# Optimization experiments

Hardware: AMD Instinct MI355X
Metric: run time of the kernel (lower is better)

## Reference

```python
import jax, jax.numpy as jnp
import numpy as np

N_EMBD = 2048
N_HEAD = 16
N_PREVS = 4
HEAD_DIM = N_EMBD // N_HEAD  # 128
B, T = 4, 2048


def setup_inputs() -> dict:
    key = jax.random.key(0)
    ks = jax.random.split(key, 3 + 2 * N_PREVS)
    inp = {
        "x": jax.random.normal(ks[0], (B, T, N_EMBD), dtype=jnp.float32),
        "w_attn": jax.random.normal(ks[1], (3 * N_EMBD, N_EMBD), dtype=jnp.float32) * 0.02,
        "w_proj": jax.random.normal(ks[2], (N_EMBD, N_EMBD), dtype=jnp.float32) * 0.02,
    }
    for i in range(N_PREVS):
        inp[f"prev_k{i}"] = jax.random.normal(ks[3 + 2 * i], (B, N_HEAD, T, HEAD_DIM), dtype=jnp.float32)
        inp[f"prev_v{i}"] = jax.random.normal(ks[4 + 2 * i], (B, N_HEAD, T, HEAD_DIM), dtype=jnp.float32)
    return inp


def _attn(q, k, v, causal):
    # q,k,v: [B, H, T, D]
    scale = 1.0 / jnp.sqrt(jnp.asarray(q.shape[-1], q.dtype))
    scores = jnp.einsum("bhqd,bhkd->bhqk", q, k) * scale
    if causal:
        mask = jnp.tril(jnp.ones((q.shape[2], k.shape[2]), dtype=bool))
        scores = jnp.where(mask, scores, jnp.finfo(scores.dtype).min)
    p = jax.nn.softmax(scores, axis=-1)
    return jnp.einsum("bhqk,bhkd->bhqd", p, v)


def reference(x, w_attn, w_proj,
              prev_k0, prev_v0, prev_k1, prev_v1,
              prev_k2, prev_v2, prev_k3, prev_v3):
    prevs = [(prev_k0, prev_v0), (prev_k1, prev_v1), (prev_k2, prev_v2), (prev_k3, prev_v3)]
    Bx, Tx, C = x.shape
    qkv = jnp.einsum("btc,fc->btf", x, w_attn)  # [B,T,3C]
    q, k, v = jnp.split(qkv, 3, axis=-1)

    def heads(t):  # [B,T,C] -> [B,H,T,D]
        return t.reshape(Bx, Tx, N_HEAD, HEAD_DIM).transpose(0, 2, 1, 3)

    q, k, v = heads(q), heads(k), heads(v)
    cur_k, cur_v = k, v

    sa_h = N_HEAD - N_PREVS
    # causal self-attention over first sa_h heads
    self_attn = _attn(q[:, :sa_h], k[:, :sa_h], v[:, :sa_h], causal=True)

    # cross-attention: head sa_h+i attends (non-causal) to head sa_h+i of prev layer i's cache
    qc = q[:, sa_h:]
    kc = jnp.stack([pk[:, sa_h + i] for i, (pk, pv) in enumerate(prevs)], axis=1)
    vc = jnp.stack([pv[:, sa_h + i] for i, (pk, pv) in enumerate(prevs)], axis=1)
    cross_attn = _attn(qc, kc, vc, causal=False)

    y = jnp.concatenate([self_attn, cross_attn], axis=1)  # [B,H,T,D]
    y = y.transpose(0, 2, 1, 3).reshape(Bx, Tx, C)
    y = jnp.einsum("btc,oc->bto", y, w_proj)
    return y, cur_k, cur_v
```

## Files before the change

### kernel.cpp

```cpp
#include <hip/hip_runtime.h>
#include <hip/hip_bf16.h>
#include <stdint.h>

typedef __attribute__((ext_vector_type(8))) short short8;
typedef __attribute__((ext_vector_type(4))) float floatx4;

#define NE 2048
#define NH 16
#define HD 128
#define SAH 12
#define BB 4
#define TT 2048
#define MM (BB*TT)
#define NQKV (3*NE)

__device__ __forceinline__ ushort f2bfu(float f){
    __hip_bfloat16 h = __float2bfloat16(f);
    union { __hip_bfloat16 h; ushort u; } c; c.h = h; return c.u;
}

__global__ void cvt_f32_bf16(const float* __restrict__ s, ushort* __restrict__ d, int n4){
    const int stride = gridDim.x * blockDim.x;
    for (int i = blockIdx.x*blockDim.x + threadIdx.x; i < n4; i += stride){
        const float4 v = ((const float4*)s)[i];
        ushort4 o;
        o.x = f2bfu(v.x); o.y = f2bfu(v.y); o.z = f2bfu(v.z); o.w = f2bfu(v.w);
        ((ushort4*)d)[i] = o;
    }
}

template<int MODE>
__global__ __launch_bounds__(256) void gemm_bt(
    const ushort* __restrict__ A, const ushort* __restrict__ Bw,
    ushort* __restrict__ Cbf, float* __restrict__ Cf,
    float* __restrict__ outK, float* __restrict__ outV,
    int N, int K)
{
    __shared__ __align__(16) ushort Alds[128*32];
    __shared__ __align__(16) ushort Blds[128*32];
    const int tid  = threadIdx.x;
    const int wave = tid >> 6, lane = tid & 63;
    const int m0 = blockIdx.y << 7, n0 = blockIdx.x << 7;
    const int wr = wave >> 1, wc = wave & 1;

    floatx4 acc[4][4];
#pragma unroll
    for (int i=0;i<4;i++)
#pragma unroll
        for (int j=0;j<4;j++) acc[i][j] = (floatx4){0.f,0.f,0.f,0.f};

    const int sr = lane >> 2, sc = (lane & 3) << 3;
    const ushort* gA = A  + (size_t)(m0 + wave*32 + sr)*K + sc;
    const ushort* gB = Bw + (size_t)(n0 + wave*32 + sr)*K + sc;
    ushort* lA = Alds + wave*32*32;
    ushort* lB = Blds + wave*32*32;
    const int fr = lane & 15, fo = (lane >> 4) << 3;

    for (int kt = 0; kt < K; kt += 32){
        __builtin_amdgcn_global_load_lds((__attribute__((address_space(1))) void*)(gA + kt),
                                         (__attribute__((address_space(3))) void*)lA, 16, 0, 0);
        __builtin_amdgcn_global_load_lds((__attribute__((address_space(1))) void*)(gA + kt + (size_t)16*K),
                                         (__attribute__((address_space(3))) void*)(lA + 16*32), 16, 0, 0);
        __builtin_amdgcn_global_load_lds((__attribute__((address_space(1))) void*)(gB + kt),
                                         (__attribute__((address_space(3))) void*)lB, 16, 0, 0);
        __builtin_amdgcn_global_load_lds((__attribute__((address_space(1))) void*)(gB + kt + (size_t)16*K),
                                         (__attribute__((address_space(3))) void*)(lB + 16*32), 16, 0, 0);
        __syncthreads();
        short8 af[4], bfb[4];
#pragma unroll
        for (int i=0;i<4;i++) af[i]  = *(const short8*)(Alds + (wr*64 + i*16 + fr)*32 + fo);
#pragma unroll
        for (int j=0;j<4;j++) bfb[j] = *(const short8*)(Blds + (wc*64 + j*16 + fr)*32 + fo);
#pragma unroll
        for (int i=0;i<4;i++)
#pragma unroll
            for (int j=0;j<4;j++)
                acc[i][j] = __builtin_amdgcn_mfma_f32_16x16x32_bf16(af[i], bfb[j], acc[i][j], 0, 0, 0);
        __syncthreads();
    }

#pragma unroll
    for (int i=0;i<4;i++){
#pragma unroll
        for (int j=0;j<4;j++){
#pragma unroll
            for (int r=0;r<4;r++){
                const int row = m0 + wr*64 + i*16 + ((lane>>4)<<2) + r;
                const int col = n0 + wc*64 + j*16 + fr;
                const float v = acc[i][j][r];
                if (MODE == 0){
                    Cf[(size_t)row*N + col] = v;
                } else {
                    Cbf[(size_t)row*NQKV + col] = f2bfu(v);
                    if (col >= NE){
                        const int b = row >> 11, t = row & (TT-1);
                        const int hd = (col - NE) & (NE-1);
                        float* dst = (col >= 2*NE) ? outV : outK;
                        dst[(((size_t)b*NH + (hd>>7))*TT + t)*HD + (hd & 127)] = v;
                    }
                }
            }
        }
    }
}

__global__ __launch_bounds__(256) void attn(
    const ushort* __restrict__ qkv, ushort* __restrict__ Y,
    const float* __restrict__ pk0, const float* __restrict__ pv0,
    const float* __restrict__ pk1, const float* __restrict__ pv1,
    const float* __restrict__ pk2, const float* __restrict__ pv2,
    const float* __restrict__ pk3, const float* __restrict__ pv3)
{
    __shared__ __align__(16) ushort Klds[32*136];
    __shared__ __align__(16) ushort Vt[128*40];
    __shared__ __align__(16) ushort Plds[4][16*40];

    const int tid  = threadIdx.x;
    const int wave = tid >> 6, lane = tid & 63;
    const int bid = blockIdx.x;
    const int qt = bid & 31;
    const int h  = (bid >> 5) & 15;
    const int b  = bid >> 9;
    const int q0 = qt << 6;
    const bool causal = (h < SAH);

    const float* pkc = nullptr; const float* pvc = nullptr;
    if (!causal){
        const int i = h - SAH;
        if      (i==0){ pkc=pk0; pvc=pv0; }
        else if (i==1){ pkc=pk1; pvc=pv1; }
        else if (i==2){ pkc=pk2; pvc=pv2; }
        else          { pkc=pk3; pvc=pv3; }
        const size_t off = ((size_t)b*NH + h)*(size_t)TT*HD;
        pkc += off; pvc += off;
    }

    const int fr = lane & 15, fo = (lane>>4) << 3;
    const int wq = q0 + wave*16;

    short8 qf[4];
    {
        const ushort* qp = qkv + (size_t)(b*TT + wq + fr)*NQKV + h*HD + fo;
#pragma unroll
        for (int kk=0;kk<4;kk++) qf[kk] = *(const short8*)(qp + kk*32);
    }

    floatx4 o[8];
#pragma unroll
    for (int dt=0; dt<8; dt++) o[dt] = (floatx4){0.f,0.f,0.f,0.f};
    float m_run[4] = {-1e30f,-1e30f,-1e30f,-1e30f};
    float l_run[4] = {0.f,0.f,0.f,0.f};

    const int srr = tid >> 3;
    const int sds = (tid & 7) << 4;
    const int nkb = causal ? ((q0 >> 5) + 2) : (TT/32);

    for (int kb = 0; kb < nkb; kb++){
        const int kstart = kb << 5;
        short8 k0v, k1v, v0v, v1v;
        if (causal){
            const ushort* sk = qkv + (size_t)(b*TT + kstart + srr)*NQKV + NE + h*HD + sds;
            const ushort* sv = sk + NE;
            k0v = *(const short8*)sk;     k1v = *(const short8*)(sk+8);
            v0v = *(const short8*)sv;     v1v = *(const short8*)(sv+8);
        } else {
            const float* sk = pkc + (size_t)(kstart + srr)*HD + sds;
            const float* sv = pvc + (size_t)(kstart + srr)*HD + sds;
            ushort* kp = (ushort*)&k0v;  ushort* kp1 = (ushort*)&k1v;
            ushort* vp = (ushort*)&v0v;  ushort* vp1 = (ushort*)&v1v;
#pragma unroll
            for (int e=0;e<8;e++){ kp[e]  = f2bfu(sk[e]);   vp[e]  = f2bfu(sv[e]); }
#pragma unroll
            for (int e=0;e<8;e++){ kp1[e] = f2bfu(sk[8+e]); vp1[e] = f2bfu(sv[8+e]); }
        }
        *(short8*)(Klds + srr*136 + sds)     = k0v;
        *(short8*)(Klds + srr*136 + sds + 8) = k1v;
        {
            const ushort* vp  = (const ushort*)&v0v;
            const ushort* vp1 = (const ushort*)&v1v;
#pragma unroll
            for (int e=0;e<8;e++) Vt[(sds+e)*40 + srr]   = vp[e];
#pragma unroll
            for (int e=0;e<8;e++) Vt[(sds+8+e)*40 + srr] = vp1[e];
        }
        __syncthreads();

        if (!causal || kstart <= wq + 15){
            floatx4 s0 = (floatx4){0.f,0.f,0.f,0.f}, s1 = (floatx4){0.f,0.f,0.f,0.f};
#pragma unroll
            for (int kk=0;kk<4;kk++){
                short8 kb0 = *(const short8*)(Klds + fr*136       + kk*32 + fo);
                short8 kb1 = *(const short8*)(Klds + (16+fr)*136  + kk*32 + fo);
                s0 = __builtin_amdgcn_mfma_f32_16x16x32_bf16(qf[kk], kb0, s0, 0,0,0);
                s1 = __builtin_amdgcn_mfma_f32_16x16x32_bf16(qf[kk], kb1, s1, 0,0,0);
            }
            const float scale = 0.08838834764831845f;
            ushort* Pw = Plds[wave];
#pragma unroll
            for (int r=0;r<4;r++){
                const int qpos = wq + ((lane>>4)<<2) + r;
                float x0 = s0[r]*scale, x1 = s1[r]*scale;
                if (causal){
                    if (kstart + fr      > qpos) x0 = -1e30f;
                    if (kstart + 16 + fr > qpos) x1 = -1e30f;
                }
                float mx = fmaxf(x0, x1);
#pragma unroll
                for (int mmk=1; mmk<16; mmk<<=1) mx = fmaxf(mx, __shfl_xor(mx, mmk));
                mx = fmaxf(mx, m_run[r]);
                const float alpha = __expf(m_run[r] - mx);
                m_run[r] = mx;
                const float p0 = __expf(x0 - mx), p1 = __expf(x1 - mx);
                float ps = p0 + p1;
#pragma unroll
                for (int mmk=1; mmk<16; mmk<<=1) ps += __shfl_xor(ps, mmk);
                l_run[r] = l_run[r]*alpha + ps;
#pragma unroll
                for (int dt=0;dt<8;dt++) o[dt][r] *= alpha;
                const int prow = ((lane>>4)<<2) + r;
                Pw[prow*40 + fr]      = f2bfu(p0);
                Pw[prow*40 + 16 + fr] = f2bfu(p1);
            }
            asm volatile("s_waitcnt lgkmcnt(0)" ::: "memory");
            short8 pf = *(const short8*)(Pw + fr*40 + fo);
#pragma unroll
            for (int dt=0;dt<8;dt++){
                short8 vf = *(const short8*)(Vt + (dt*16 + fr)*40 + fo);
                o[dt] = __builtin_amdgcn_mfma_f32_16x16x32_bf16(pf, vf, o[dt], 0,0,0);
            }
        }
        __syncthreads();
    }

    float inv[4];
#pragma unroll
    for (int r=0;r<4;r++) inv[r] = 1.0f / l_run[r];
#pragma unroll
    for (int dt=0;dt<8;dt++){
#pragma unroll
        for (int r=0;r<4;r++){
            const int q = wq + ((lane>>4)<<2) + r;
            const int d = dt*16 + fr;
            Y[(size_t)(b*TT + q)*NE + h*HD + d] = f2bfu(o[dt][r]*inv[r]);
        }
    }
}

extern "C" void kernel_launch(void* const* d_in, const int* in_sizes, int n_in,
                              void* d_out, int out_size, void* d_ws, size_t ws_size,
                              hipStream_t stream)
{
    const float* x      = (const float*)d_in[0];
    const float* w_attn = (const float*)d_in[1];
    const float* w_proj = (const float*)d_in[2];
    const float* pk0 = (const float*)d_in[3];
    const float* pv0 = (const float*)d_in[4];
    const float* pk1 = (const float*)d_in[5];
    const float* pv1 = (const float*)d_in[6];
    const float* pk2 = (const float*)d_in[7];
    const float* pv2 = (const float*)d_in[8];
    const float* pk3 = (const float*)d_in[9];
    const float* pv3 = (const float*)d_in[10];

    float* outY = (float*)d_out;
    float* outK = outY + (size_t)MM*NE;
    float* outV = outK + (size_t)MM*NE;

    char* w = (char*)d_ws;
    ushort* x_bf   = (ushort*)(w);
    ushort* wa_bf  = (ushort*)(w + 33554432);
    ushort* wp_bf  = (ushort*)(w + 58720256);
    ushort* qkv_bf = (ushort*)(w + 67108864);
    ushort* y_bf   = (ushort*)(w + 167772160);

    cvt_f32_bf16<<<2048, 256, 0, stream>>>(x,      x_bf,  MM*NE/4);
    cvt_f32_bf16<<<2048, 256, 0, stream>>>(w_attn, wa_bf, NQKV*NE/4);
    cvt_f32_bf16<<<1024, 256, 0, stream>>>(w_proj, wp_bf, NE*NE/4);

    gemm_bt<1><<<dim3(NQKV/128, MM/128), 256, 0, stream>>>(
        x_bf, wa_bf, qkv_bf, nullptr, outK, outV, NQKV, NE);

    attn<<<BB*NH*(TT/64), 256, 0, stream>>>(
        qkv_bf, y_bf, pk0, pv0, pk1, pv1, pk2, pv2, pk3, pv3);

    gemm_bt<0><<<dim3(NE/128, MM/128), 256, 0, stream>>>(
        y_bf, wp_bf, nullptr, outY, nullptr, nullptr, NE, NE);
}
```

Before: 1.507 ms.

## Pretranspose V and preconvert cross KV, use 64-key tiles with direct LDS loads

Adds pre-pass kernels that convert the cross-attention K cache to bf16 and write V (self and cross) pre-transposed into workspace buffers reused from the earlier conversion buffers. The attention kernel now processes 64-key blocks, fills LDS with global_load_lds using an XOR swizzle instead of per-element transposing stores, and drops the per-block fp32-to-bf16 conversion of the cross caches. This targets uncoalesced scalar LDS transposes, redundant conversions repeated by each query tile, and sync overhead. The cost is extra kernel launches and transpose passes through global memory. The w_proj conversion moves after attention so its buffer can hold the K cache.

```diff
diff --git a/kernel.cpp b/kernel.cpp
--- a/kernel.cpp
+++ b/kernel.cpp
@@ -13,11 +13,14 @@
 #define TT 2048
 #define MM (BB*TT)
 #define NQKV (3*NE)
+#define KBLK 64
 
 __device__ __forceinline__ ushort f2bfu(float f){
     __hip_bfloat16 h = __float2bfloat16(f);
     union { __hip_bfloat16 h; ushort u; } c; c.h = h; return c.u;
 }
+
+__device__ __forceinline__ int swz(int r){ return (((r>>3)&3)<<1) ^ (r&7); }
 
 __global__ void cvt_f32_bf16(const float* __restrict__ s, ushort* __restrict__ d, int n4){
     const int stride = gridDim.x * blockDim.x;
@@ -27,6 +30,53 @@
         o.x = f2bfu(v.x); o.y = f2bfu(v.y); o.z = f2bfu(v.z); o.w = f2bfu(v.w);
         ((ushort4*)d)[i] = o;
     }
+}
+
+__global__ void kc_cvt(const float* __restrict__ pk0, const float* __restrict__ pk1,
+                       const float* __restrict__ pk2, const float* __restrict__ pk3,
+                       ushort* __restrict__ kc){
+    const int bh2 = blockIdx.y;
+    const int i = bh2 & 3, b = bh2 >> 2;
+    const float* src = (i==0?pk0 : i==1?pk1 : i==2?pk2 : pk3)
+                     + (size_t)(b*NH + SAH + i)*TT*HD;
+    const int idx = (blockIdx.x*256 + threadIdx.x)*8;
+    float4 a0 = *(const float4*)(src + idx);
+    float4 a1 = *(const float4*)(src + idx + 4);
+    ushort* dst = kc + (size_t)bh2*TT*HD + idx;
+    ushort4 o0, o1;
+    o0.x=f2bfu(a0.x); o0.y=f2bfu(a0.y); o0.z=f2bfu(a0.z); o0.w=f2bfu(a0.w);
+    o1.x=f2bfu(a1.x); o1.y=f2bfu(a1.y); o1.z=f2bfu(a1.z); o1.w=f2bfu(a1.w);
+    *(ushort4*)dst = o0; *(ushort4*)(dst+4) = o1;
+}
+
+__global__ void vt_cross_k(const float* __restrict__ pv0, const float* __restrict__ pv1,
+                           const float* __restrict__ pv2, const float* __restrict__ pv3,
+                           ushort* __restrict__ vtC){
+    const int bh2 = blockIdx.z;
+    const int i = bh2 & 3, b = bh2 >> 2;
+    const int db = blockIdx.y;
+    const int t  = blockIdx.x*256 + threadIdx.x;
+    const float* src = (i==0?pv0 : i==1?pv1 : i==2?pv2 : pv3)
+                     + ((size_t)(b*NH + SAH + i)*TT + t)*HD + db*8;
+    float4 a0 = *(const float4*)src;
+    float4 a1 = *(const float4*)(src + 4);
+    float vals[8] = {a0.x,a0.y,a0.z,a0.w,a1.x,a1.y,a1.z,a1.w};
+#pragma unroll
+    for (int e=0;e<8;e++)
+        vtC[((size_t)bh2*HD + db*8 + e)*TT + t] = f2bfu(vals[e]);
+}
+
+__global__ void vt_self_k(const ushort* __restrict__ qkv, ushort* __restrict__ vtS){
+    const int bh = blockIdx.z;
+    const int b = bh/12, h = bh%12;
+    const int db = blockIdx.y;
+    const int t  = blockIdx.x*256 + threadIdx.x;
+    const ushort* src = qkv + (size_t)(b*TT + t)*NQKV + 2*NE + h*HD + db*8;
+    short8 v = *(const short8*)src;
+    const ushort* vp = (const ushort*)&v;
+#pragma unroll
+    for (int e=0;e<8;e++)
+        vtS[((size_t)bh*HD + db*8 + e)*TT + t] = vp[e];
 }
 
 template<int MODE>
@@ -104,19 +154,18 @@
     }
 }
 
-__global__ __launch_bounds__(256) void attn(
-    const ushort* __restrict__ qkv, ushort* __restrict__ Y,
-    const float* __restrict__ pk0, const float* __restrict__ pv0,
-    const float* __restrict__ pk1, const float* __restrict__ pv1,
-    const float* __restrict__ pk2, const float* __restrict__ pv2,
-    const float* __restrict__ pk3, const float* __restrict__ pv3)
+__global__ __launch_bounds__(256) void attn2(
+    const ushort* __restrict__ qkv, const ushort* __restrict__ kc,
+    const ushort* __restrict__ vtS, const ushort* __restrict__ vtC,
+    ushort* __restrict__ Y)
 {
-    __shared__ __align__(16) ushort Klds[32*136];
-    __shared__ __align__(16) ushort Vt[128*40];
-    __shared__ __align__(16) ushort Plds[4][16*40];
+    __shared__ __align__(16) ushort Klds[64*128];
+    __shared__ __align__(16) ushort Vlds[128*64];
+    __shared__ __align__(16) ushort Plds[4][16*64];
 
     const int tid  = threadIdx.x;
     const int wave = tid >> 6, lane = tid & 63;
+    const int fr = lane & 15, g = lane >> 4;
     const int bid = blockIdx.x;
     const int qt = bid & 31;
     const int h  = (bid >> 5) & 15;
@@ -124,25 +173,34 @@
     const int q0 = qt << 6;
     const bool causal = (h < SAH);
 
-    const float* pkc = nullptr; const float* pvc = nullptr;
-    if (!causal){
+    const ushort* Kbase; size_t strideK; const ushort* Vbase;
+    if (causal){
+        Kbase = qkv + (size_t)b*TT*NQKV + NE + h*HD;  strideK = NQKV;
+        Vbase = vtS + (size_t)(b*12 + h)*HD*TT;
+    } else {
         const int i = h - SAH;
-        if      (i==0){ pkc=pk0; pvc=pv0; }
-        else if (i==1){ pkc=pk1; pvc=pv1; }
-        else if (i==2){ pkc=pk2; pvc=pv2; }
-        else          { pkc=pk3; pvc=pv3; }
-        const size_t off = ((size_t)b*NH + h)*(size_t)TT*HD;
-        pkc += off; pvc += off;
-    }
-
-    const int fr = lane & 15, fo = (lane>>4) << 3;
+        Kbase = kc  + (size_t)(b*4 + i)*TT*HD;        strideK = HD;
+        Vbase = vtC + (size_t)(b*4 + i)*HD*TT;
+    }
     const int wq = q0 + wave*16;
 
     short8 qf[4];
     {
-        const ushort* qp = qkv + (size_t)(b*TT + wq + fr)*NQKV + h*HD + fo;
+        const ushort* qp = qkv + (size_t)(b*TT + wq + fr)*NQKV + h*HD + g*8;
 #pragma unroll
         for (int kk=0;kk<4;kk++) qf[kk] = *(const short8*)(qp + kk*32);
+    }
+
+    size_t koff[4], voff[4];
+#pragma unroll
+    for (int i=0;i<4;i++){
+        const int row = wave*16 + i*4 + (lane>>4);
+        koff[i] = (size_t)row*strideK + (size_t)(((lane & 15) ^ swz(row)) << 3);
+    }
+#pragma unroll
+    for (int i=0;i<4;i++){
+        const int row = wave*32 + i*8 + (lane>>3);
+        voff[i] = (size_t)row*TT + (size_t)(((lane & 7) ^ swz(row)) << 3);
     }
 
     floatx4 o[8];
@@ -151,85 +209,89 @@
     float m_run[4] = {-1e30f,-1e30f,-1e30f,-1e30f};
     float l_run[4] = {0.f,0.f,0.f,0.f};
 
-    const int srr = tid >> 3;
-    const int sds = (tid & 7) << 4;
-    const int nkb = causal ? ((q0 >> 5) + 2) : (TT/32);
+    const float scale = 0.08838834764831845f;
+    const int nkb = causal ? (qt + 1) : (TT/KBLK);
 
     for (int kb = 0; kb < nkb; kb++){
-        const int kstart = kb << 5;
-        short8 k0v, k1v, v0v, v1v;
-        if (causal){
-            const ushort* sk = qkv + (size_t)(b*TT + kstart + srr)*NQKV + NE + h*HD + sds;
-            const ushort* sv = sk + NE;
-            k0v = *(const short8*)sk;     k1v = *(const short8*)(sk+8);
-            v0v = *(const short8*)sv;     v1v = *(const short8*)(sv+8);
-        } else {
-            const float* sk = pkc + (size_t)(kstart + srr)*HD + sds;
-            const float* sv = pvc + (size_t)(kstart + srr)*HD + sds;
-            ushort* kp = (ushort*)&k0v;  ushort* kp1 = (ushort*)&k1v;
-            ushort* vp = (ushort*)&v0v;  ushort* vp1 = (ushort*)&v1v;
-#pragma unroll
-            for (int e=0;e<8;e++){ kp[e]  = f2bfu(sk[e]);   vp[e]  = f2bfu(sv[e]); }
-#pragma unroll
-            for (int e=0;e<8;e++){ kp1[e] = f2bfu(sk[8+e]); vp1[e] = f2bfu(sv[8+e]); }
-        }
-        *(short8*)(Klds + srr*136 + sds)     = k0v;
-        *(short8*)(Klds + srr*136 + sds + 8) = k1v;
+        const int kstart = kb << 6;
+#pragma unroll
+        for (int i=0;i<4;i++)
+            __builtin_amdgcn_global_load_lds(
+                (__attribute__((address_space(1))) void*)(Kbase + (size_t)kstart*strideK + koff[i]),
+                (__attribute__((address_space(3))) void*)(Klds + (wave*4+i)*512), 16, 0, 0);
+#pragma unroll
+        for (int i=0;i<4;i++)
+            __builtin_amdgcn_global_load_lds(
+                (__attribute__((address_space(1))) void*)(Vbase + (size_t)kstart + voff[i]),
+                (__attribute__((address_space(3))) void*)(Vlds + (wave*4+i)*512), 16, 0, 0);
+        __syncthreads();
+
+        floatx4 sA[4];
+#pragma unroll
+        for (int j=0;j<4;j++) sA[j] = (floatx4){0.f,0.f,0.f,0.f};
+#pragma unroll
+        for (int j=0;j<4;j++){
+            const int row = 16*j + fr;
+            const int sR = swz(row);
+#pragma unroll
+            for (int kk=0;kk<4;kk++){
+                const short8 kf = *(const short8*)(Klds + row*128 + (((kk*4+g) ^ sR)<<3));
+                sA[j] = __builtin_amdgcn_mfma_f32_16x16x32_bf16(qf[kk], kf, sA[j], 0,0,0);
+            }
+        }
+
+        const bool domask = causal && (kstart + 63 > wq);
+        ushort* Pw = Plds[wave];
+#pragma unroll
+        for (int r=0;r<4;r++){
+            float xs[4];
+#pragma unroll
+            for (int j=0;j<4;j++) xs[j] = sA[j][r]*scale;
+            if (domask){
+                const int qpos = wq + 4*g + r;
+#pragma unroll
+                for (int j=0;j<4;j++)
+                    if (kstart + 16*j + fr > qpos) xs[j] = -1e30f;
+            }
+            float mx = fmaxf(fmaxf(xs[0],xs[1]), fmaxf(xs[2],xs[3]));
+#pragma unroll
+            for (int d=1; d<16; d<<=1) mx = fmaxf(mx, __shfl_xor(mx, d));
+            const float mn = fmaxf(m_run[r], mx);
+            const float alpha = __expf(m_run[r] - mn);
+            m_run[r] = mn;
+            float p[4]; float ps = 0.f;
+#pragma unroll
+            for (int j=0;j<4;j++){ p[j] = __expf(xs[j]-mn); ps += p[j]; }
+#pragma unroll
+            for (int d=1; d<16; d<<=1) ps += __shfl_xor(ps, d);
+            l_run[r] = l_run[r]*alpha + ps;
+#pragma unroll
+            for (int dt=0;dt<8;dt++) o[dt][r] *= alpha;
+            const int q = 4*g + r;
+            const int sq = swz(q);
+#pragma unroll
+            for (int j=0;j<4;j++)
+                Pw[q*64 + (((2*j + (fr>>3)) ^ sq)<<3) + (fr&7)] = f2bfu(p[j]);
+        }
+
+        short8 pa[2];
         {
-            const ushort* vp  = (const ushort*)&v0v;
-            const ushort* vp1 = (const ushort*)&v1v;
-#pragma unroll
-            for (int e=0;e<8;e++) Vt[(sds+e)*40 + srr]   = vp[e];
-#pragma unroll
-            for (int e=0;e<8;e++) Vt[(sds+8+e)*40 + srr] = vp1[e];
+            const int sF = swz(fr);
+#pragma unroll
+            for (int ks=0;ks<2;ks++)
+                pa[ks] = *(const short8*)(Pw + fr*64 + (((ks*4+g) ^ sF)<<3));
+        }
+#pragma unroll
+        for (int dt=0;dt<8;dt++){
+            const int row = dt*16 + fr;
+            const int sR = swz(row);
+#pragma unroll
+            for (int ks=0;ks<2;ks++){
+                const short8 vf = *(const short8*)(Vlds + row*64 + (((ks*4+g) ^ sR)<<3));
+                o[dt] = __builtin_amdgcn_mfma_f32_16x16x32_bf16(pa[ks], vf, o[dt], 0,0,0);
+            }
         }
         __syncthreads();
-
-        if (!causal || kstart <= wq + 15){
-            floatx4 s0 = (floatx4){0.f,0.f,0.f,0.f}, s1 = (floatx4){0.f,0.f,0.f,0.f};
-#pragma unroll
-            for (int kk=0;kk<4;kk++){
-                short8 kb0 = *(const short8*)(Klds + fr*136       + kk*32 + fo);
-                short8 kb1 = *(const short8*)(Klds + (16+fr)*136  + kk*32 + fo);
-                s0 = __builtin_amdgcn_mfma_f32_16x16x32_bf16(qf[kk], kb0, s0, 0,0,0);
-                s1 = __builtin_amdgcn_mfma_f32_16x16x32_bf16(qf[kk], kb1, s1, 0,0,0);
-            }
-            const float scale = 0.08838834764831845f;
-            ushort* Pw = Plds[wave];
-#pragma unroll
-            for (int r=0;r<4;r++){
-                const int qpos = wq + ((lane>>4)<<2) + r;
-                float x0 = s0[r]*scale, x1 = s1[r]*scale;
-                if (causal){
-                    if (kstart + fr      > qpos) x0 = -1e30f;
-                    if (kstart + 16 + fr > qpos) x1 = -1e30f;
-                }
-                float mx = fmaxf(x0, x1);
-#pragma unroll
-                for (int mmk=1; mmk<16; mmk<<=1) mx = fmaxf(mx, __shfl_xor(mx, mmk));
-                mx = fmaxf(mx, m_run[r]);
-                const float alpha = __expf(m_run[r] - mx);
-                m_run[r] = mx;
-                const float p0 = __expf(x0 - mx), p1 = __expf(x1 - mx);
-                float ps = p0 + p1;
-#pragma unroll
-                for (int mmk=1; mmk<16; mmk<<=1) ps += __shfl_xor(ps, mmk);
-                l_run[r] = l_run[r]*alpha + ps;
-#pragma unroll
-                for (int dt=0;dt<8;dt++) o[dt][r] *= alpha;
-                const int prow = ((lane>>4)<<2) + r;
-                Pw[prow*40 + fr]      = f2bfu(p0);
-                Pw[prow*40 + 16 + fr] = f2bfu(p1);
-            }
-            asm volatile("s_waitcnt lgkmcnt(0)" ::: "memory");
-            short8 pf = *(const short8*)(Pw + fr*40 + fo);
-#pragma unroll
-            for (int dt=0;dt<8;dt++){
-                short8 vf = *(const short8*)(Vt + (dt*16 + fr)*40 + fo);
-                o[dt] = __builtin_amdgcn_mfma_f32_16x16x32_bf16(pf, vf, o[dt], 0,0,0);
-            }
-        }
-        __syncthreads();
     }
 
     float inv[4];
@@ -239,7 +301,7 @@
     for (int dt=0;dt<8;dt++){
 #pragma unroll
         for (int r=0;r<4;r++){
-            const int q = wq + ((lane>>4)<<2) + r;
+            const int q = wq + 4*g + r;
             const int d = dt*16 + fr;
             Y[(size_t)(b*TT + q)*NE + h*HD + d] = f2bfu(o[dt][r]*inv[r]);
         }
@@ -272,16 +334,24 @@
     ushort* wp_bf  = (ushort*)(w + 58720256);
     ushort* qkv_bf = (ushort*)(w + 67108864);
     ushort* y_bf   = (ushort*)(w + 167772160);
+    ushort* kc     = wp_bf;
+    ushort* vtS    = x_bf;
+    ushort* vtC    = wa_bf;
 
     cvt_f32_bf16<<<2048, 256, 0, stream>>>(x,      x_bf,  MM*NE/4);
     cvt_f32_bf16<<<2048, 256, 0, stream>>>(w_attn, wa_bf, NQKV*NE/4);
-    cvt_f32_bf16<<<1024, 256, 0, stream>>>(w_proj, wp_bf, NE*NE/4);
+
+    kc_cvt<<<dim3(128,16), 256, 0, stream>>>(pk0, pk1, pk2, pk3, kc);
 
     gemm_bt<1><<<dim3(NQKV/128, MM/128), 256, 0, stream>>>(
         x_bf, wa_bf, qkv_bf, nullptr, outK, outV, NQKV, NE);
 
-    attn<<<BB*NH*(TT/64), 256, 0, stream>>>(
-        qkv_bf, y_bf, pk0, pv0, pk1, pv1, pk2, pv2, pk3, pv3);
+    vt_self_k<<<dim3(8,16,48), 256, 0, stream>>>(qkv_bf, vtS);
+    vt_cross_k<<<dim3(8,16,16), 256, 0, stream>>>(pv0, pv1, pv2, pv3, vtC);
+
+    attn2<<<BB*NH*(TT/64), 256, 0, stream>>>(qkv_bf, kc, vtS, vtC, y_bf);
+
+    cvt_f32_bf16<<<1024, 256, 0, stream>>>(w_proj, wp_bf, NE*NE/4);
 
     gemm_bt<0><<<dim3(NE/128, MM/128), 256, 0, stream>>>(
         y_bf, wp_bf, nullptr, outY, nullptr, nullptr, NE, NE);
```

After: 1.253 ms. 16.8% less time.
